# Kernel optimization log

Measured on AMD Instinct MI355X. Metric: run time of the kernel, lower is better.

## Reference

```python
import jax, jax.numpy as jnp
import numpy as np

K = 16  # knn_graph k, loop=True (self included since d(i,i)=0 is minimal)


def _knn_idx(pos, k):
    # exact kNN via pairwise squared distances; [N, k] neighbor indices
    sq = jnp.sum(pos * pos, axis=-1)
    d2 = sq[:, None] + sq[None, :] - 2.0 * (pos @ pos.T)  # [N, N]
    _, idx = jax.lax.top_k(-d2, k)
    return idx


def _pointnet_conv(x, pos, idx, Wa, ba, Wb, bb):
    # PointNetConv: msg = MLP(concat(x_j, pos_j - pos_i)), max-aggregate over neighbors
    rel = pos[idx] - pos[:, None, :]                    # [N, K, 3]
    m = jnp.concatenate([x[idx], rel], axis=-1)          # [N, K, Cin+3]
    h = jax.nn.relu(m @ Wa + ba) @ Wb + bb               # [N, K, Cout]
    return jnp.max(h, axis=1)                            # [N, Cout]


def setup_inputs() -> dict:
    key = jax.random.key(0)
    ks = jax.random.split(key, 13)
    N = 8192
    c1, c2, c3 = 64, 64, 128
    s = lambda fi: 1.0 / np.sqrt(fi)
    pos = jax.random.normal(ks[0], (N, 3), dtype=jnp.float32)
    return {
        "pos": pos,
        "W1a": jax.random.normal(ks[1], (3 + 3, c1), jnp.float32) * s(6),
        "b1a": jnp.zeros((c1,), jnp.float32),
        "W1b": jax.random.normal(ks[2], (c1, c1), jnp.float32) * s(c1),
        "b1b": jnp.zeros((c1,), jnp.float32),
        "W2a": jax.random.normal(ks[3], (c1 + 3, c2), jnp.float32) * s(c1 + 3),
        "b2a": jnp.zeros((c2,), jnp.float32),
        "W2b": jax.random.normal(ks[4], (c2, c2), jnp.float32) * s(c2),
        "b2b": jnp.zeros((c2,), jnp.float32),
        "W3a": jax.random.normal(ks[5], (c2 + 3, c3), jnp.float32) * s(c2 + 3),
        "b3a": jnp.zeros((c3,), jnp.float32),
        "W3b": jax.random.normal(ks[6], (c3, c3), jnp.float32) * s(c3),
        "b3b": jnp.zeros((c3,), jnp.float32),
    }


def reference(pos, W1a, b1a, W1b, b1b, W2a, b2a, W2b, b2b, W3a, b3a, W3b, b3b):
    idx = _knn_idx(pos, K)
    h1 = jax.nn.relu(_pointnet_conv(pos, pos, idx, W1a, b1a, W1b, b1b))
    h2 = jax.nn.relu(_pointnet_conv(h1, pos, idx, W2a, b2a, W2b, b2b))
    h3 = jax.nn.relu(_pointnet_conv(h2, pos, idx, W3a, b3a, W3b, b3b))
    return (h1, h2, h3)
```

## Files before the change

kernel.cpp:

```cpp
#include <hip/hip_runtime.h>
#include <math.h>

#define N_PTS 8192
#define KNN 16

typedef __attribute__((ext_vector_type(8))) short bf16x8;
typedef __attribute__((ext_vector_type(4))) float f32x4v;

__device__ __forceinline__ unsigned short f2bf(float f)
{
    unsigned u = __float_as_uint(f);
    u = u + 0x7fffu + ((u >> 16) & 1u);
    return (unsigned short)(u >> 16);
}
__device__ __forceinline__ unsigned pack2(float a, float b)
{
    return (unsigned)f2bf(a) | ((unsigned)f2bf(b) << 16);
}
__device__ __forceinline__ float rfl(float x)
{
    return __int_as_float(__builtin_amdgcn_readfirstlane(__float_as_int(x)));
}

__global__ __launch_bounds__(256) void prep_all(
    const float* __restrict__ pos, float4* __restrict__ pos4,
    const float* __restrict__ w1a, const float* __restrict__ w1b,
    const float* __restrict__ w2a, const float* __restrict__ w2b,
    const float* __restrict__ w3a, const float* __restrict__ w3b,
    uint4* __restrict__ dst)
{
    const int b = blockIdx.x;
    if (b < 88) {
        if (threadIdx.x >= 64) return;
        const float* Ws[6] = {w1a, w1b, w2a, w2b, w3a, w3b};
        const int Kd[6] = {6, 64, 67, 64, 67, 128};
        const int Nd[6] = {64, 64, 64, 64, 128, 128};
        const int start[7] = {0, 4, 12, 24, 32, 56, 88};
        int m = 0;
        while (b >= start[m + 1]) ++m;
        const int f  = b - start[m];
        const int NT = Nd[m] / 16;
        const int ks = f / NT, nt = f % NT;
        const int lane = threadIdx.x;
        const int c  = nt * 16 + (lane & 15);
        const int k0 = ks * 32 + (lane >> 4) * 8;
        const int K = Kd[m], N = Nd[m];
        const float* W = Ws[m];
        float v[8];
#pragma unroll
        for (int j = 0; j < 8; ++j) {
            const int kk = k0 + j;
            v[j] = (kk < K) ? W[kk * N + c] : 0.0f;
        }
        uint4 o;
        o.x = pack2(v[0], v[1]); o.y = pack2(v[2], v[3]);
        o.z = pack2(v[4], v[5]); o.w = pack2(v[6], v[7]);
        dst[b * 64 + lane] = o;
    } else {
        const int i = (b - 88) * 256 + threadIdx.x;
        const float x = pos[i * 3 + 0];
        const float y = pos[i * 3 + 1];
        const float z = pos[i * 3 + 2];
        pos4[i] = make_float4(x, y, z, fmaf(x, x, fmaf(y, y, z * z)));
    }
}

__device__ __forceinline__ unsigned sortkey(const float d2)
{
    unsigned u = __float_as_uint(d2);
    u ^= (unsigned)((int)u >> 31) | 0x80000000u;
    return u;
}
__device__ __forceinline__ float unkey(unsigned k)
{
    const unsigned u = (k & 0x80000000u) ? (k ^ 0x80000000u) : ~k;
    return __uint_as_float(u);
}

constexpr int CAP   = 128;
constexpr int QB    = 16;
constexpr int TILE  = 1024;
constexpr int NTL   = N_PTS / TILE;

__device__ __forceinline__ void stage_tile(const float4* src, float4* dst)
{
    __builtin_amdgcn_global_load_lds(
        (const __attribute__((address_space(1))) void*)src,
        (__attribute__((address_space(3))) void*)dst, 16, 0, 0);
}

__global__ __launch_bounds__(512) void knn_kernel(const float4* __restrict__ pos4,
                                                  int* __restrict__ idx_out)
{
    __shared__ float4 tile[2][TILE];
    __shared__ unsigned minkey[QB][64];
    __shared__ float Ts[QB];
    __shared__ unsigned long long surv[QB][CAP];
    __shared__ int scnt[QB];

    const int tid   = threadIdx.x;
    const int w     = tid >> 6;
    const int lane  = tid & 63;
    const int qbase = blockIdx.x * QB;

    if (tid < QB) scnt[tid] = 0;
    reinterpret_cast<unsigned*>(minkey)[tid]       = 0xFFFFFFFFu;
    reinterpret_cast<unsigned*>(minkey)[tid + 512] = 0xFFFFFFFFu;

    float qx[QB], qy[QB], qz[QB];
#pragma unroll
    for (int qi = 0; qi < QB; ++qi) {
        const float4 qp = pos4[qbase + qi];
        qx[qi] = rfl(-2.0f * qp.x);
        qy[qi] = rfl(-2.0f * qp.y);
        qz[qi] = rfl(-2.0f * qp.z);
    }

    const float4* src = pos4 + w * 128 + lane;
    float4* dst0 = &tile[0][w * 128];
    float4* dst1 = &tile[1][w * 128];

    float mn[QB];
#pragma unroll
    for (int qi = 0; qi < QB; ++qi) mn[qi] = 1e30f;

    stage_tile(src,      dst0);
    stage_tile(src + 64, dst0 + 64);
    __syncthreads();
#pragma unroll 1
    for (int t = 0; t < NTL - 1; ++t) {
        float4* nd = (t & 1) ? dst0 : dst1;
        stage_tile(src + (t + 1) * TILE,      nd);
        stage_tile(src + (t + 1) * TILE + 64, nd + 64);
        asm volatile("s_waitcnt vmcnt(2)" ::: "memory");
        __builtin_amdgcn_sched_barrier(0);
        const float4 p0 = tile[t & 1][w * 128 + lane];
        const float4 p1 = tile[t & 1][w * 128 + 64 + lane];
#pragma unroll
        for (int qi = 0; qi < QB; ++qi) {
            const float s0 = fmaf(qx[qi], p0.x, fmaf(qy[qi], p0.y, fmaf(qz[qi], p0.z, p0.w)));
            const float s1 = fmaf(qx[qi], p1.x, fmaf(qy[qi], p1.y, fmaf(qz[qi], p1.z, p1.w)));
            mn[qi] = fminf(mn[qi], fminf(s0, s1));
        }
    }
    {
        asm volatile("s_waitcnt vmcnt(0)" ::: "memory");
        __builtin_amdgcn_sched_barrier(0);
        const int t = NTL - 1;
        const float4 p0 = tile[t & 1][w * 128 + lane];
        const float4 p1 = tile[t & 1][w * 128 + 64 + lane];
#pragma unroll
        for (int qi = 0; qi < QB; ++qi) {
            const float s0 = fmaf(qx[qi], p0.x, fmaf(qy[qi], p0.y, fmaf(qz[qi], p0.z, p0.w)));
            const float s1 = fmaf(qx[qi], p1.x, fmaf(qy[qi], p1.y, fmaf(qz[qi], p1.z, p1.w)));
            mn[qi] = fminf(mn[qi], fminf(s0, s1));
        }
    }
#pragma unroll
    for (int qi = 0; qi < QB; ++qi) atomicMin(&minkey[qi][lane], sortkey(mn[qi]));
    __syncthreads();

#pragma unroll
    for (int k = 0; k < 2; ++k) {
        const int q = w * 2 + k;
        unsigned v = minkey[q][lane];
#pragma unroll
        for (int kk = 2; kk <= 64; kk <<= 1)
#pragma unroll
            for (int j = kk >> 1; j > 0; j >>= 1) {
                const unsigned o = __shfl_xor(v, j);
                const bool up = ((lane & kk) == 0);
                const bool lo = ((lane & j) == 0);
                v = (up == lo) ? min(v, o) : max(v, o);
            }
        if (lane == 15) Ts[q] = unkey(v);
    }
    __syncthreads();

    float T[QB];
#pragma unroll
    for (int qi = 0; qi < QB; ++qi) T[qi] = rfl(Ts[qi]);

    stage_tile(src,      dst0);
    stage_tile(src + 64, dst0 + 64);
#pragma unroll 1
    for (int t = 0; t < NTL - 1; ++t) {
        float4* nd = (t & 1) ? dst0 : dst1;
        stage_tile(src + (t + 1) * TILE,      nd);
        stage_tile(src + (t + 1) * TILE + 64, nd + 64);
        asm volatile("s_waitcnt vmcnt(2)" ::: "memory");
        __builtin_amdgcn_sched_barrier(0);
#pragma unroll
        for (int u = 0; u < 2; ++u) {
            const float4 p = tile[t & 1][w * 128 + u * 64 + lane];
            const int j = t * TILE + w * 128 + u * 64 + lane;
#pragma unroll
            for (int qi = 0; qi < QB; ++qi) {
                const float s = fmaf(qx[qi], p.x, fmaf(qy[qi], p.y, fmaf(qz[qi], p.z, p.w)));
                if (s <= T[qi]) {
                    const int slot = atomicAdd(&scnt[qi], 1);
                    if (slot < CAP)
                        surv[qi][slot] = ((unsigned long long)sortkey(s) << 32) | (unsigned)j;
                }
            }
        }
    }
    {
        asm volatile("s_waitcnt vmcnt(0)" ::: "memory");
        __builtin_amdgcn_sched_barrier(0);
        const int t = NTL - 1;
#pragma unroll
        for (int u = 0; u < 2; ++u) {
            const float4 p = tile[t & 1][w * 128 + u * 64 + lane];
            const int j = t * TILE + w * 128 + u * 64 + lane;
#pragma unroll
            for (int qi = 0; qi < QB; ++qi) {
                const float s = fmaf(qx[qi], p.x, fmaf(qy[qi], p.y, fmaf(qz[qi], p.z, p.w)));
                if (s <= T[qi]) {
                    const int slot = atomicAdd(&scnt[qi], 1);
                    if (slot < CAP)
                        surv[qi][slot] = ((unsigned long long)sortkey(s) << 32) | (unsigned)j;
                }
            }
        }
    }
    __syncthreads();

#pragma unroll
    for (int k = 0; k < 2; ++k) {
        const int q = w * 2 + k;
        const int n = min(scnt[q], CAP);
        const unsigned long long k0 = (lane < n) ? surv[q][lane] : ~0ull;
        const unsigned long long k1 = (lane + 64 < n) ? surv[q][lane + 64] : ~0ull;
        int r0 = 0, r1 = 0;
#pragma unroll 4
        for (int e = 0; e < n; ++e) {
            const unsigned long long ke = surv[q][e];
            r0 += (ke < k0) ? 1 : 0;
            r1 += (ke < k1) ? 1 : 0;
        }
        if (lane < n && r0 < KNN)
            idx_out[(qbase + q) * KNN + r0] = (int)(unsigned)(k0 & 0xFFFFFFFFu);
        if (lane + 64 < n && r1 < KNN)
            idx_out[(qbase + q) * KNN + r1] = (int)(unsigned)(k1 & 0xFFFFFFFFu);
    }
}

template <int CIN, int CMID, int COUT, int WM, int WN>
__global__ __launch_bounds__(256) void conv_mfma(
    const float* __restrict__ x, const float* __restrict__ pos,
    const int* __restrict__ idx,
    const uint4* __restrict__ fA, const float* __restrict__ ba,
    const uint4* __restrict__ fB, const float* __restrict__ bb,
    float* __restrict__ out)
{
    constexpr int PB  = 8, M = 128;
    constexpr int K1  = (CIN + 3 + 31) & ~31;
    constexpr int KS1 = K1 / 32;
    constexpr int KP1 = K1 + 8;
    constexpr int KS2 = CMID / 32;
    constexpr int KP2 = CMID + 8;
    constexpr int NT  = COUT / 16;
    constexpr int NTW = NT / WN;
    constexpr int MFW = (M / 16) / WM;
    constexpr int MSGS = M * KP1;
    constexpr int HBS  = M * KP2;
    constexpr int BUFS = (MSGS > HBS) ? MSGS : HBS;

    __shared__ int nbr[M];
    __shared__ __align__(16) unsigned short buf[BUFS];

    const int tid  = threadIdx.x;
    const int lane = tid & 63;
    const int w    = tid >> 6;
    const int wm   = w / WN, wn = w % WN;
    const int i0   = blockIdx.x * PB;

    if (tid < M) nbr[tid] = idx[i0 * KNN + tid];
    __syncthreads();

    if constexpr (CIN == 3) {
        if (tid < M) {
            const int row = tid, p = row >> 4, j = nbr[row];
            const float ax = pos[j * 3 + 0], ay = pos[j * 3 + 1], az = pos[j * 3 + 2];
            const float bx = pos[(i0 + p) * 3 + 0], by = pos[(i0 + p) * 3 + 1],
                        bz = pos[(i0 + p) * 3 + 2];
            uint4 c0;
            c0.x = pack2(ax, ay);
            c0.y = pack2(az, ax - bx);
            c0.z = pack2(ay - by, az - bz);
            c0.w = 0u;
            *reinterpret_cast<uint4*>(&buf[row * KP1 + 0])  = c0;
            const uint4 z = make_uint4(0, 0, 0, 0);
            *reinterpret_cast<uint4*>(&buf[row * KP1 + 8])  = z;
            *reinterpret_cast<uint4*>(&buf[row * KP1 + 16]) = z;
            *reinterpret_cast<uint4*>(&buf[row * KP1 + 24]) = z;
        }
    } else {
        const int row = tid >> 1, hh = tid & 1;
        const int j = nbr[row];
        const float* xr = x + j * CIN + hh * 32;
#pragma unroll
        for (int cc = 0; cc < 32; cc += 8) {
            const float4 f0 = *reinterpret_cast<const float4*>(xr + cc);
            const float4 f1 = *reinterpret_cast<const float4*>(xr + cc + 4);
            uint4 o;
            o.x = pack2(f0.x, f0.y); o.y = pack2(f0.z, f0.w);
            o.z = pack2(f1.x, f1.y); o.w = pack2(f1.z, f1.w);
            *reinterpret_cast<uint4*>(&buf[row * KP1 + hh * 32 + cc]) = o;
        }
        if (hh) {
            const int p = row >> 4;
            const float rx = pos[j * 3 + 0] - pos[(i0 + p) * 3 + 0];
            const float ry = pos[j * 3 + 1] - pos[(i0 + p) * 3 + 1];
            const float rz = pos[j * 3 + 2] - pos[(i0 + p) * 3 + 2];
            uint4 c0;
            c0.x = pack2(rx, ry);
            c0.y = pack2(rz, 0.0f);
            c0.z = 0u; c0.w = 0u;
            *reinterpret_cast<uint4*>(&buf[row * KP1 + 64]) = c0;
            const uint4 z = make_uint4(0, 0, 0, 0);
            *reinterpret_cast<uint4*>(&buf[row * KP1 + 72]) = z;
            *reinterpret_cast<uint4*>(&buf[row * KP1 + 80]) = z;
            *reinterpret_cast<uint4*>(&buf[row * KP1 + 88]) = z;
        }
    }
    __syncthreads();

    f32x4v acc[MFW][NTW];
    {
        uint4 b1[KS1][NTW];
#pragma unroll
        for (int ks = 0; ks < KS1; ++ks)
#pragma unroll
            for (int nt = 0; nt < NTW; ++nt)
                b1[ks][nt] = fA[(ks * NT + wn * NTW + nt) * 64 + lane];

#pragma unroll
        for (int mf = 0; mf < MFW; ++mf)
#pragma unroll
            for (int nt = 0; nt < NTW; ++nt) acc[mf][nt] = (f32x4v)0.0f;

#pragma unroll
        for (int mf = 0; mf < MFW; ++mf) {
            bf16x8 a[KS1];
#pragma unroll
            for (int ks = 0; ks < KS1; ++ks)
                a[ks] = *reinterpret_cast<const bf16x8*>(
                    &buf[((wm * MFW + mf) * 16 + (lane & 15)) * KP1 + ks * 32 + (lane >> 4) * 8]);
#pragma unroll
            for (int nt = 0; nt < NTW; ++nt)
#pragma unroll
                for (int ks = 0; ks < KS1; ++ks)
                    acc[mf][nt] = __builtin_amdgcn_mfma_f32_16x16x32_bf16(
                        a[ks], __builtin_bit_cast(bf16x8, b1[ks][nt]), acc[mf][nt], 0, 0, 0);
        }
    }
    __syncthreads();

    {
        float bav[NTW];
#pragma unroll
        for (int nt = 0; nt < NTW; ++nt) bav[nt] = ba[(wn * NTW + nt) * 16 + (lane & 15)];
#pragma unroll
        for (int mf = 0; mf < MFW; ++mf)
#pragma unroll
            for (int nt = 0; nt < NTW; ++nt)
#pragma unroll
                for (int r = 0; r < 4; ++r) {
                    const float v = fmaxf(acc[mf][nt][r] + bav[nt], 0.0f);
                    buf[((wm * MFW + mf) * 16 + (lane >> 4) * 4 + r) * KP2 +
                        (wn * NTW + nt) * 16 + (lane & 15)] = f2bf(v);
                }
    }
    __syncthreads();

    {
        uint4 b2[KS2][NTW];
#pragma unroll
        for (int ks = 0; ks < KS2; ++ks)
#pragma unroll
            for (int nt = 0; nt < NTW; ++nt)
                b2[ks][nt] = fB[(ks * NT + wn * NTW + nt) * 64 + lane];

        f32x4v acc2[MFW][NTW];
#pragma unroll
        for (int mf = 0; mf < MFW; ++mf)
#pragma unroll
            for (int nt = 0; nt < NTW; ++nt) acc2[mf][nt] = (f32x4v)0.0f;

#pragma unroll
        for (int mf = 0; mf < MFW; ++mf) {
            bf16x8 a[KS2];
#pragma unroll
            for (int ks = 0; ks < KS2; ++ks)
                a[ks] = *reinterpret_cast<const bf16x8*>(
                    &buf[((wm * MFW + mf) * 16 + (lane & 15)) * KP2 + ks * 32 + (lane >> 4) * 8]);
#pragma unroll
            for (int nt = 0; nt < NTW; ++nt)
#pragma unroll
                for (int ks = 0; ks < KS2; ++ks)
                    acc2[mf][nt] = __builtin_amdgcn_mfma_f32_16x16x32_bf16(
                        a[ks], __builtin_bit_cast(bf16x8, b2[ks][nt]), acc2[mf][nt], 0, 0, 0);
        }

        float bbv[NTW];
#pragma unroll
        for (int nt = 0; nt < NTW; ++nt) bbv[nt] = bb[(wn * NTW + nt) * 16 + (lane & 15)];

#pragma unroll
        for (int mf = 0; mf < MFW; ++mf)
#pragma unroll
            for (int nt = 0; nt < NTW; ++nt) {
                const f32x4v t = acc2[mf][nt];
                float m0 = fmaxf(fmaxf(t[0], t[1]), fmaxf(t[2], t[3]));
                m0 = fmaxf(m0, __shfl_xor(m0, 16));
                m0 = fmaxf(m0, __shfl_xor(m0, 32));
                const float v = fmaxf(m0 + bbv[nt], 0.0f);
                if (lane < 16)
                    out[(i0 + wm * MFW + mf) * COUT + (wn * NTW + nt) * 16 + lane] = v;
            }
    }
}

extern "C" void kernel_launch(void* const* d_in, const int* in_sizes, int n_in,
                              void* d_out, int out_size, void* d_ws, size_t ws_size,
                              hipStream_t stream)
{
    const float* pos = (const float*)d_in[0];
    const float* W1a = (const float*)d_in[1];
    const float* b1a = (const float*)d_in[2];
    const float* W1b = (const float*)d_in[3];
    const float* b1b = (const float*)d_in[4];
    const float* W2a = (const float*)d_in[5];
    const float* b2a = (const float*)d_in[6];
    const float* W2b = (const float*)d_in[7];
    const float* b2b = (const float*)d_in[8];
    const float* W3a = (const float*)d_in[9];
    const float* b3a = (const float*)d_in[10];
    const float* W3b = (const float*)d_in[11];
    const float* b3b = (const float*)d_in[12];

    float* out = (float*)d_out;
    float* h1 = out;
    float* h2 = out + N_PTS * 64;
    float* h3 = out + N_PTS * 128;

    int*   idx     = (int*)d_ws;
    uint4* wsFrags = (uint4*)((char*)d_ws + N_PTS * KNN * 4);

    float4* pos4 = (float4*)h3;

    prep_all<<<120, 256, 0, stream>>>(pos, pos4, W1a, W1b, W2a, W2b, W3a, W3b, wsFrags);
    knn_kernel<<<N_PTS / QB, 512, 0, stream>>>(pos4, idx);

    const uint4* fW1a = wsFrags + 0 * 64;
    const uint4* fW1b = wsFrags + 4 * 64;
    const uint4* fW2a = wsFrags + 12 * 64;
    const uint4* fW2b = wsFrags + 24 * 64;
    const uint4* fW3a = wsFrags + 32 * 64;
    const uint4* fW3b = wsFrags + 56 * 64;

    conv_mfma<3, 64, 64, 4, 1><<<N_PTS / 8, 256, 0, stream>>>(
        pos, pos, idx, fW1a, b1a, fW1b, b1b, h1);
    conv_mfma<64, 64, 64, 4, 1><<<N_PTS / 8, 256, 0, stream>>>(
        h1, pos, idx, fW2a, b2a, fW2b, b2b, h2);
    conv_mfma<64, 128, 128, 2, 2><<<N_PTS / 8, 256, 0, stream>>>(
        h2, pos, idx, fW3a, b3a, fW3b, b3b, h3);
}
```

Measured before the change: 74.24 us.

## Halve kNN query block, triple-buffer tiles, and early-out candidate filtering

Cuts the kNN kernel to 8 queries and 512-point tiles per block, which doubles the block count and adds a launch-bounds occupancy hint. Tile staging moves from double to triple buffering, so loads run two tiles ahead of compute. The filtering pass now computes all query scores first and branches only when some query passes its threshold, aiming to skip the per-query atomic path in the common case. In exchange, the position array is streamed twice per block across twice as many blocks, so global/L2 traffic doubles.

```diff
diff --git a/kernel.cpp b/kernel.cpp
--- a/kernel.cpp
+++ b/kernel.cpp
@@ -78,8 +78,8 @@
 }
 
 constexpr int CAP   = 128;
-constexpr int QB    = 16;
-constexpr int TILE  = 1024;
+constexpr int QB    = 8;
+constexpr int TILE  = 512;
 constexpr int NTL   = N_PTS / TILE;
 
 __device__ __forceinline__ void stage_tile(const float4* src, float4* dst)
@@ -89,10 +89,10 @@
         (__attribute__((address_space(3))) void*)dst, 16, 0, 0);
 }
 
-__global__ __launch_bounds__(512) void knn_kernel(const float4* __restrict__ pos4,
-                                                  int* __restrict__ idx_out)
-{
-    __shared__ float4 tile[2][TILE];
+__global__ __launch_bounds__(512, 8) void knn_kernel(const float4* __restrict__ pos4,
+                                                     int* __restrict__ idx_out)
+{
+    __shared__ float4 tile[3][TILE];
     __shared__ unsigned minkey[QB][64];
     __shared__ float Ts[QB];
     __shared__ unsigned long long surv[QB][CAP];
@@ -104,8 +104,7 @@
     const int qbase = blockIdx.x * QB;
 
     if (tid < QB) scnt[tid] = 0;
-    reinterpret_cast<unsigned*>(minkey)[tid]       = 0xFFFFFFFFu;
-    reinterpret_cast<unsigned*>(minkey)[tid + 512] = 0xFFFFFFFFu;
+    reinterpret_cast<unsigned*>(minkey)[tid] = 0xFFFFFFFFu;
 
     float qx[QB], qy[QB], qz[QB];
 #pragma unroll
@@ -116,54 +115,46 @@
         qz[qi] = rfl(-2.0f * qp.z);
     }
 
-    const float4* src = pos4 + w * 128 + lane;
-    float4* dst0 = &tile[0][w * 128];
-    float4* dst1 = &tile[1][w * 128];
+    const float4* src = pos4 + w * 64 + lane;
 
     float mn[QB];
 #pragma unroll
     for (int qi = 0; qi < QB; ++qi) mn[qi] = 1e30f;
 
-    stage_tile(src,      dst0);
-    stage_tile(src + 64, dst0 + 64);
+    stage_tile(src + 0 * TILE, &tile[0][w * 64]);
+    stage_tile(src + 1 * TILE, &tile[1][w * 64]);
     __syncthreads();
 #pragma unroll 1
-    for (int t = 0; t < NTL - 1; ++t) {
-        float4* nd = (t & 1) ? dst0 : dst1;
-        stage_tile(src + (t + 1) * TILE,      nd);
-        stage_tile(src + (t + 1) * TILE + 64, nd + 64);
+    for (int t = 0; t < NTL - 2; ++t) {
+        stage_tile(src + (t + 2) * TILE, &tile[(t + 2) % 3][w * 64]);
         asm volatile("s_waitcnt vmcnt(2)" ::: "memory");
         __builtin_amdgcn_sched_barrier(0);
-        const float4 p0 = tile[t & 1][w * 128 + lane];
-        const float4 p1 = tile[t & 1][w * 128 + 64 + lane];
+        const float4 p = tile[t % 3][w * 64 + lane];
 #pragma unroll
         for (int qi = 0; qi < QB; ++qi) {
-            const float s0 = fmaf(qx[qi], p0.x, fmaf(qy[qi], p0.y, fmaf(qz[qi], p0.z, p0.w)));
-            const float s1 = fmaf(qx[qi], p1.x, fmaf(qy[qi], p1.y, fmaf(qz[qi], p1.z, p1.w)));
-            mn[qi] = fminf(mn[qi], fminf(s0, s1));
-        }
-    }
+            const float s = fmaf(qx[qi], p.x, fmaf(qy[qi], p.y, fmaf(qz[qi], p.z, p.w)));
+            mn[qi] = fminf(mn[qi], s);
+        }
+    }
+#pragma unroll
+    for (int tt = 0; tt < 2; ++tt) {
+        if (tt == 0) asm volatile("s_waitcnt vmcnt(1)" ::: "memory");
+        else         asm volatile("s_waitcnt vmcnt(0)" ::: "memory");
+        __builtin_amdgcn_sched_barrier(0);
+        const int t = NTL - 2 + tt;
+        const float4 p = tile[t % 3][w * 64 + lane];
+#pragma unroll
+        for (int qi = 0; qi < QB; ++qi) {
+            const float s = fmaf(qx[qi], p.x, fmaf(qy[qi], p.y, fmaf(qz[qi], p.z, p.w)));
+            mn[qi] = fminf(mn[qi], s);
+        }
+    }
+#pragma unroll
+    for (int qi = 0; qi < QB; ++qi) atomicMin(&minkey[qi][lane], sortkey(mn[qi]));
+    __syncthreads();
+
     {
-        asm volatile("s_waitcnt vmcnt(0)" ::: "memory");
-        __builtin_amdgcn_sched_barrier(0);
-        const int t = NTL - 1;
-        const float4 p0 = tile[t & 1][w * 128 + lane];
-        const float4 p1 = tile[t & 1][w * 128 + 64 + lane];
-#pragma unroll
-        for (int qi = 0; qi < QB; ++qi) {
-            const float s0 = fmaf(qx[qi], p0.x, fmaf(qy[qi], p0.y, fmaf(qz[qi], p0.z, p0.w)));
-            const float s1 = fmaf(qx[qi], p1.x, fmaf(qy[qi], p1.y, fmaf(qz[qi], p1.z, p1.w)));
-            mn[qi] = fminf(mn[qi], fminf(s0, s1));
-        }
-    }
-#pragma unroll
-    for (int qi = 0; qi < QB; ++qi) atomicMin(&minkey[qi][lane], sortkey(mn[qi]));
-    __syncthreads();
-
-#pragma unroll
-    for (int k = 0; k < 2; ++k) {
-        const int q = w * 2 + k;
-        unsigned v = minkey[q][lane];
+        unsigned v = minkey[w][lane];
 #pragma unroll
         for (int kk = 2; kk <= 64; kk <<= 1)
 #pragma unroll
@@ -173,7 +164,7 @@
                 const bool lo = ((lane & j) == 0);
                 v = (up == lo) ? min(v, o) : max(v, o);
             }
-        if (lane == 15) Ts[q] = unkey(v);
+        if (lane == 15) Ts[w] = unkey(v);
     }
     __syncthreads();
 
@@ -181,54 +172,61 @@
 #pragma unroll
     for (int qi = 0; qi < QB; ++qi) T[qi] = rfl(Ts[qi]);
 
-    stage_tile(src,      dst0);
-    stage_tile(src + 64, dst0 + 64);
+    stage_tile(src + 0 * TILE, &tile[0][w * 64]);
+    stage_tile(src + 1 * TILE, &tile[1][w * 64]);
 #pragma unroll 1
-    for (int t = 0; t < NTL - 1; ++t) {
-        float4* nd = (t & 1) ? dst0 : dst1;
-        stage_tile(src + (t + 1) * TILE,      nd);
-        stage_tile(src + (t + 1) * TILE + 64, nd + 64);
+    for (int t = 0; t < NTL - 2; ++t) {
+        stage_tile(src + (t + 2) * TILE, &tile[(t + 2) % 3][w * 64]);
         asm volatile("s_waitcnt vmcnt(2)" ::: "memory");
         __builtin_amdgcn_sched_barrier(0);
-#pragma unroll
-        for (int u = 0; u < 2; ++u) {
-            const float4 p = tile[t & 1][w * 128 + u * 64 + lane];
-            const int j = t * TILE + w * 128 + u * 64 + lane;
-#pragma unroll
-            for (int qi = 0; qi < QB; ++qi) {
-                const float s = fmaf(qx[qi], p.x, fmaf(qy[qi], p.y, fmaf(qz[qi], p.z, p.w)));
-                if (s <= T[qi]) {
+        const float4 p = tile[t % 3][w * 64 + lane];
+        const int j = t * TILE + w * 64 + lane;
+        float s[QB];
+        bool hit = false;
+#pragma unroll
+        for (int qi = 0; qi < QB; ++qi) {
+            s[qi] = fmaf(qx[qi], p.x, fmaf(qy[qi], p.y, fmaf(qz[qi], p.z, p.w)));
+            hit = hit | (s[qi] <= T[qi]);
+        }
+        if (__builtin_expect(hit, 0)) {
+#pragma unroll
+            for (int qi = 0; qi < QB; ++qi)
+                if (s[qi] <= T[qi]) {
                     const int slot = atomicAdd(&scnt[qi], 1);
                     if (slot < CAP)
-                        surv[qi][slot] = ((unsigned long long)sortkey(s) << 32) | (unsigned)j;
+                        surv[qi][slot] = ((unsigned long long)sortkey(s[qi]) << 32) | (unsigned)j;
                 }
-            }
-        }
-    }
-    {
-        asm volatile("s_waitcnt vmcnt(0)" ::: "memory");
+        }
+    }
+#pragma unroll
+    for (int tt = 0; tt < 2; ++tt) {
+        if (tt == 0) asm volatile("s_waitcnt vmcnt(1)" ::: "memory");
+        else         asm volatile("s_waitcnt vmcnt(0)" ::: "memory");
         __builtin_amdgcn_sched_barrier(0);
-        const int t = NTL - 1;
-#pragma unroll
-        for (int u = 0; u < 2; ++u) {
-            const float4 p = tile[t & 1][w * 128 + u * 64 + lane];
-            const int j = t * TILE + w * 128 + u * 64 + lane;
-#pragma unroll
-            for (int qi = 0; qi < QB; ++qi) {
-                const float s = fmaf(qx[qi], p.x, fmaf(qy[qi], p.y, fmaf(qz[qi], p.z, p.w)));
-                if (s <= T[qi]) {
+        const int t = NTL - 2 + tt;
+        const float4 p = tile[t % 3][w * 64 + lane];
+        const int j = t * TILE + w * 64 + lane;
+        float s[QB];
+        bool hit = false;
+#pragma unroll
+        for (int qi = 0; qi < QB; ++qi) {
+            s[qi] = fmaf(qx[qi], p.x, fmaf(qy[qi], p.y, fmaf(qz[qi], p.z, p.w)));
+            hit = hit | (s[qi] <= T[qi]);
+        }
+        if (__builtin_expect(hit, 0)) {
+#pragma unroll
+            for (int qi = 0; qi < QB; ++qi)
+                if (s[qi] <= T[qi]) {
                     const int slot = atomicAdd(&scnt[qi], 1);
                     if (slot < CAP)
-                        surv[qi][slot] = ((unsigned long long)sortkey(s) << 32) | (unsigned)j;
+                        surv[qi][slot] = ((unsigned long long)sortkey(s[qi]) << 32) | (unsigned)j;
                 }
-            }
-        }
-    }
-    __syncthreads();
-
-#pragma unroll
-    for (int k = 0; k < 2; ++k) {
-        const int q = w * 2 + k;
+        }
+    }
+    __syncthreads();
+
+    {
+        const int q = w;
         const int n = min(scnt[q], CAP);
         const unsigned long long k0 = (lane < n) ? surv[q][lane] : ~0ull;
         const unsigned long long k1 = (lane + 64 < n) ? surv[q][lane + 64] : ~0ull;
```

Measured after the change: 77.99 us. 5.0% more time.

## Precompute per-point first-layer projections and fuse them into previous conv epilogue

Applied to the files above, without the earlier changes.

Splits the first linear layer of each PointNetConv algebraically into a per-source-point term (x_j and pos_j times Wa, plus bias) and a per-center term (pos_i times the rel rows of Wa). The per-point term is computed once per point, in prep for layer 1 and in the previous conv's epilogue for later layers, and stored as bf16. The conv kernel then only gathers these vectors, subtracts the center term and applies relu. This removes the first MFMA GEMM over N*K messages, adding a scalar FMA epilogue, extra scratch buffers placed in output and workspace, and extra bf16 rounding of the intermediate.

```diff
diff --git a/kernel.cpp b/kernel.cpp
--- a/kernel.cpp
+++ b/kernel.cpp
@@ -17,6 +17,10 @@
 {
     return (unsigned)f2bf(a) | ((unsigned)f2bf(b) << 16);
 }
+__device__ __forceinline__ float bf2f(unsigned short h)
+{
+    return __uint_as_float((unsigned)h << 16);
+}
 __device__ __forceinline__ float rfl(float x)
 {
     return __int_as_float(__builtin_amdgcn_readfirstlane(__float_as_int(x)));
@@ -24,18 +28,19 @@
 
 __global__ __launch_bounds__(256) void prep_all(
     const float* __restrict__ pos, float4* __restrict__ pos4,
-    const float* __restrict__ w1a, const float* __restrict__ w1b,
-    const float* __restrict__ w2a, const float* __restrict__ w2b,
-    const float* __restrict__ w3a, const float* __restrict__ w3b,
+    unsigned short* __restrict__ v1,
+    const float* __restrict__ w1a, const float* __restrict__ b1a,
+    const float* __restrict__ w1b, const float* __restrict__ w2b,
+    const float* __restrict__ w3b,
     uint4* __restrict__ dst)
 {
     const int b = blockIdx.x;
-    if (b < 88) {
+    if (b < 48) {
         if (threadIdx.x >= 64) return;
-        const float* Ws[6] = {w1a, w1b, w2a, w2b, w3a, w3b};
-        const int Kd[6] = {6, 64, 67, 64, 67, 128};
-        const int Nd[6] = {64, 64, 64, 64, 128, 128};
-        const int start[7] = {0, 4, 12, 24, 32, 56, 88};
+        const float* Ws[3] = {w1b, w2b, w3b};
+        const int Kd[3] = {64, 64, 128};
+        const int Nd[3] = {64, 64, 128};
+        const int start[4] = {0, 8, 16, 48};
         int m = 0;
         while (b >= start[m + 1]) ++m;
         const int f  = b - start[m];
@@ -44,24 +49,43 @@
         const int lane = threadIdx.x;
         const int c  = nt * 16 + (lane & 15);
         const int k0 = ks * 32 + (lane >> 4) * 8;
-        const int K = Kd[m], N = Nd[m];
+        const int N = Nd[m];
         const float* W = Ws[m];
         float v[8];
 #pragma unroll
-        for (int j = 0; j < 8; ++j) {
-            const int kk = k0 + j;
-            v[j] = (kk < K) ? W[kk * N + c] : 0.0f;
-        }
+        for (int j = 0; j < 8; ++j) v[j] = W[(k0 + j) * N + c];
         uint4 o;
         o.x = pack2(v[0], v[1]); o.y = pack2(v[2], v[3]);
         o.z = pack2(v[4], v[5]); o.w = pack2(v[6], v[7]);
         dst[b * 64 + lane] = o;
-    } else {
-        const int i = (b - 88) * 256 + threadIdx.x;
+    } else if (b < 80) {
+        const int i = (b - 48) * 256 + threadIdx.x;
         const float x = pos[i * 3 + 0];
         const float y = pos[i * 3 + 1];
         const float z = pos[i * 3 + 2];
         pos4[i] = make_float4(x, y, z, fmaf(x, x, fmaf(y, y, z * z)));
+    } else {
+        const int i = (b - 80) * 256 + threadIdx.x;
+        const float px = pos[i * 3 + 0], py = pos[i * 3 + 1], pz = pos[i * 3 + 2];
+#pragma unroll
+        for (int c8 = 0; c8 < 64; c8 += 8) {
+            unsigned o[4];
+#pragma unroll
+            for (int d2 = 0; d2 < 4; ++d2) {
+                float r[2];
+#pragma unroll
+                for (int e = 0; e < 2; ++e) {
+                    const int c = c8 + d2 * 2 + e;
+                    float acc = b1a[c];
+                    acc = fmaf(px, w1a[0 * 64 + c] + w1a[3 * 64 + c], acc);
+                    acc = fmaf(py, w1a[1 * 64 + c] + w1a[4 * 64 + c], acc);
+                    acc = fmaf(pz, w1a[2 * 64 + c] + w1a[5 * 64 + c], acc);
+                    r[e] = acc;
+                }
+                o[d2] = pack2(r[0], r[1]);
+            }
+            *reinterpret_cast<uint4*>(v1 + i * 64 + c8) = make_uint4(o[0], o[1], o[2], o[3]);
+        }
     }
 }
 
@@ -233,7 +257,6 @@
         const unsigned long long k0 = (lane < n) ? surv[q][lane] : ~0ull;
         const unsigned long long k1 = (lane + 64 < n) ? surv[q][lane + 64] : ~0ull;
         int r0 = 0, r1 = 0;
-#pragma unroll 4
         for (int e = 0; e < n; ++e) {
             const unsigned long long ke = surv[q][e];
             r0 += (ke < k0) ? 1 : 0;
@@ -246,29 +269,25 @@
     }
 }
 
-template <int CIN, int CMID, int COUT, int WM, int WN>
-__global__ __launch_bounds__(256) void conv_mfma(
-    const float* __restrict__ x, const float* __restrict__ pos,
+template <int CMID, int COUT, int WM, int WN, int VNEXT>
+__global__ __launch_bounds__(256) void conv_fused(
+    const unsigned short* __restrict__ v, const float* __restrict__ pos,
     const int* __restrict__ idx,
-    const uint4* __restrict__ fA, const float* __restrict__ ba,
+    const float* __restrict__ WaRel,
     const uint4* __restrict__ fB, const float* __restrict__ bb,
-    float* __restrict__ out)
+    const float* __restrict__ Wnext, const float* __restrict__ bnext,
+    float* __restrict__ out, unsigned short* __restrict__ vout)
 {
     constexpr int PB  = 8, M = 128;
-    constexpr int K1  = (CIN + 3 + 31) & ~31;
-    constexpr int KS1 = K1 / 32;
-    constexpr int KP1 = K1 + 8;
+    constexpr int KP2 = CMID + 8;
     constexpr int KS2 = CMID / 32;
-    constexpr int KP2 = CMID + 8;
     constexpr int NT  = COUT / 16;
     constexpr int NTW = NT / WN;
     constexpr int MFW = (M / 16) / WM;
-    constexpr int MSGS = M * KP1;
-    constexpr int HBS  = M * KP2;
-    constexpr int BUFS = (MSGS > HBS) ? MSGS : HBS;
 
     __shared__ int nbr[M];
-    __shared__ __align__(16) unsigned short buf[BUFS];
+    __shared__ float ubuf[PB][CMID];
+    __shared__ __align__(16) unsigned short hbuf[M * KP2];
 
     const int tid  = threadIdx.x;
     const int lane = tid & 63;
@@ -277,104 +296,40 @@
     const int i0   = blockIdx.x * PB;
 
     if (tid < M) nbr[tid] = idx[i0 * KNN + tid];
-    __syncthreads();
-
-    if constexpr (CIN == 3) {
-        if (tid < M) {
-            const int row = tid, p = row >> 4, j = nbr[row];
-            const float ax = pos[j * 3 + 0], ay = pos[j * 3 + 1], az = pos[j * 3 + 2];
-            const float bx = pos[(i0 + p) * 3 + 0], by = pos[(i0 + p) * 3 + 1],
-                        bz = pos[(i0 + p) * 3 + 2];
-            uint4 c0;
-            c0.x = pack2(ax, ay);
-            c0.y = pack2(az, ax - bx);
-            c0.z = pack2(ay - by, az - bz);
-            c0.w = 0u;
-            *reinterpret_cast<uint4*>(&buf[row * KP1 + 0])  = c0;
-            const uint4 z = make_uint4(0, 0, 0, 0);
-            *reinterpret_cast<uint4*>(&buf[row * KP1 + 8])  = z;
-            *reinterpret_cast<uint4*>(&buf[row * KP1 + 16]) = z;
-            *reinterpret_cast<uint4*>(&buf[row * KP1 + 24]) = z;
-        }
-    } else {
+    for (int e = tid; e < PB * CMID; e += 256) {
+        const int pt = e / CMID, c = e % CMID;
+        float u = pos[(i0 + pt) * 3 + 0] * WaRel[c];
+        u = fmaf(pos[(i0 + pt) * 3 + 1], WaRel[CMID + c], u);
+        u = fmaf(pos[(i0 + pt) * 3 + 2], WaRel[2 * CMID + c], u);
+        ubuf[pt][c] = u;
+    }
+    __syncthreads();
+
+    {
         const int row = tid >> 1, hh = tid & 1;
-        const int j = nbr[row];
-        const float* xr = x + j * CIN + hh * 32;
-#pragma unroll
-        for (int cc = 0; cc < 32; cc += 8) {
-            const float4 f0 = *reinterpret_cast<const float4*>(xr + cc);
-            const float4 f1 = *reinterpret_cast<const float4*>(xr + cc + 4);
-            uint4 o;
-            o.x = pack2(f0.x, f0.y); o.y = pack2(f0.z, f0.w);
-            o.z = pack2(f1.x, f1.y); o.w = pack2(f1.z, f1.w);
-            *reinterpret_cast<uint4*>(&buf[row * KP1 + hh * 32 + cc]) = o;
-        }
-        if (hh) {
-            const int p = row >> 4;
-            const float rx = pos[j * 3 + 0] - pos[(i0 + p) * 3 + 0];
-            const float ry = pos[j * 3 + 1] - pos[(i0 + p) * 3 + 1];
-            const float rz = pos[j * 3 + 2] - pos[(i0 + p) * 3 + 2];
-            uint4 c0;
-            c0.x = pack2(rx, ry);
-            c0.y = pack2(rz, 0.0f);
-            c0.z = 0u; c0.w = 0u;
-            *reinterpret_cast<uint4*>(&buf[row * KP1 + 64]) = c0;
-            const uint4 z = make_uint4(0, 0, 0, 0);
-            *reinterpret_cast<uint4*>(&buf[row * KP1 + 72]) = z;
-            *reinterpret_cast<uint4*>(&buf[row * KP1 + 80]) = z;
-            *reinterpret_cast<uint4*>(&buf[row * KP1 + 88]) = z;
-        }
-    }
-    __syncthreads();
-
-    f32x4v acc[MFW][NTW];
-    {
-        uint4 b1[KS1][NTW];
-#pragma unroll
-        for (int ks = 0; ks < KS1; ++ks)
-#pragma unroll
-            for (int nt = 0; nt < NTW; ++nt)
-                b1[ks][nt] = fA[(ks * NT + wn * NTW + nt) * 64 + lane];
-
-#pragma unroll
-        for (int mf = 0; mf < MFW; ++mf)
-#pragma unroll
-            for (int nt = 0; nt < NTW; ++nt) acc[mf][nt] = (f32x4v)0.0f;
-
-#pragma unroll
-        for (int mf = 0; mf < MFW; ++mf) {
-            bf16x8 a[KS1];
-#pragma unroll
-            for (int ks = 0; ks < KS1; ++ks)
-                a[ks] = *reinterpret_cast<const bf16x8*>(
-                    &buf[((wm * MFW + mf) * 16 + (lane & 15)) * KP1 + ks * 32 + (lane >> 4) * 8]);
-#pragma unroll
-            for (int nt = 0; nt < NTW; ++nt)
-#pragma unroll
-                for (int ks = 0; ks < KS1; ++ks)
-                    acc[mf][nt] = __builtin_amdgcn_mfma_f32_16x16x32_bf16(
-                        a[ks], __builtin_bit_cast(bf16x8, b1[ks][nt]), acc[mf][nt], 0, 0, 0);
-        }
-    }
-    __syncthreads();
-
-    {
-        float bav[NTW];
-#pragma unroll
-        for (int nt = 0; nt < NTW; ++nt) bav[nt] = ba[(wn * NTW + nt) * 16 + (lane & 15)];
-#pragma unroll
-        for (int mf = 0; mf < MFW; ++mf)
-#pragma unroll
-            for (int nt = 0; nt < NTW; ++nt)
-#pragma unroll
-                for (int r = 0; r < 4; ++r) {
-                    const float v = fmaxf(acc[mf][nt][r] + bav[nt], 0.0f);
-                    buf[((wm * MFW + mf) * 16 + (lane >> 4) * 4 + r) * KP2 +
-                        (wn * NTW + nt) * 16 + (lane & 15)] = f2bf(v);
-                }
-    }
-    __syncthreads();
-
+        const int j = nbr[row], pt = row >> 4;
+        const int cb = hh * (CMID / 2);
+#pragma unroll
+        for (int cc = 0; cc < CMID / 2; cc += 8) {
+            const uint4 vv = *reinterpret_cast<const uint4*>(v + j * CMID + cb + cc);
+            const unsigned dw[4] = {vv.x, vv.y, vv.z, vv.w};
+            unsigned o[4];
+#pragma unroll
+            for (int d2 = 0; d2 < 4; ++d2) {
+                const int c = cb + cc + d2 * 2;
+                const float flo = __uint_as_float(dw[d2] << 16);
+                const float fhi = __uint_as_float(dw[d2] & 0xffff0000u);
+                const float rlo = fmaxf(flo - ubuf[pt][c],     0.0f);
+                const float rhi = fmaxf(fhi - ubuf[pt][c + 1], 0.0f);
+                o[d2] = pack2(rlo, rhi);
+            }
+            *reinterpret_cast<uint4*>(&hbuf[row * KP2 + cb + cc]) =
+                make_uint4(o[0], o[1], o[2], o[3]);
+        }
+    }
+    __syncthreads();
+
+    float outv[MFW][NTW];
     {
         uint4 b2[KS2][NTW];
 #pragma unroll
@@ -395,7 +350,7 @@
 #pragma unroll
             for (int ks = 0; ks < KS2; ++ks)
                 a[ks] = *reinterpret_cast<const bf16x8*>(
-                    &buf[((wm * MFW + mf) * 16 + (lane & 15)) * KP2 + ks * 32 + (lane >> 4) * 8]);
+                    &hbuf[((wm * MFW + mf) * 16 + (lane & 15)) * KP2 + ks * 32 + (lane >> 4) * 8]);
 #pragma unroll
             for (int nt = 0; nt < NTW; ++nt)
 #pragma unroll
@@ -416,10 +371,52 @@
                 float m0 = fmaxf(fmaxf(t[0], t[1]), fmaxf(t[2], t[3]));
                 m0 = fmaxf(m0, __shfl_xor(m0, 16));
                 m0 = fmaxf(m0, __shfl_xor(m0, 32));
-                const float v = fmaxf(m0 + bbv[nt], 0.0f);
-                if (lane < 16)
-                    out[(i0 + wm * MFW + mf) * COUT + (wn * NTW + nt) * 16 + lane] = v;
-            }
+                outv[mf][nt] = fmaxf(m0 + bbv[nt], 0.0f);
+            }
+    }
+    __syncthreads();
+
+#pragma unroll
+    for (int mf = 0; mf < MFW; ++mf)
+#pragma unroll
+        for (int nt = 0; nt < NTW; ++nt) {
+            if (lane < 16) {
+                const int pt = wm * MFW + mf;
+                const int c  = (wn * NTW + nt) * 16 + lane;
+                out[(i0 + pt) * COUT + c] = outv[mf][nt];
+                if constexpr (VNEXT > 0) hbuf[pt * KP2 + c] = f2bf(outv[mf][nt]);
+            }
+        }
+
+    if constexpr (VNEXT > 0) {
+        __syncthreads();
+        constexpr int CPT = VNEXT / 32;
+        const int pt = tid >> 5;
+        const int c0 = (tid & 31) * CPT;
+        float acc[CPT];
+#pragma unroll
+        for (int e = 0; e < CPT; ++e) acc[e] = bnext[c0 + e];
+        for (int k = 0; k < COUT; ++k) {
+            const float hk = bf2f(hbuf[pt * KP2 + k]);
+#pragma unroll
+            for (int e = 0; e < CPT; ++e)
+                acc[e] = fmaf(hk, Wnext[k * VNEXT + c0 + e], acc[e]);
+        }
+#pragma unroll
+        for (int d = 0; d < 3; ++d) {
+            const float pd = pos[(i0 + pt) * 3 + d];
+#pragma unroll
+            for (int e = 0; e < CPT; ++e)
+                acc[e] = fmaf(pd, Wnext[(COUT + d) * VNEXT + c0 + e], acc[e]);
+        }
+        if constexpr (CPT == 2) {
+            *reinterpret_cast<unsigned*>(vout + (i0 + pt) * VNEXT + c0) = pack2(acc[0], acc[1]);
+        } else {
+            uint2 o;
+            o.x = pack2(acc[0], acc[1]);
+            o.y = pack2(acc[2], acc[3]);
+            *reinterpret_cast<uint2*>(vout + (i0 + pt) * VNEXT + c0) = o;
+        }
     }
 }
 
@@ -446,25 +443,25 @@
     float* h2 = out + N_PTS * 64;
     float* h3 = out + N_PTS * 128;
 
-    int*   idx     = (int*)d_ws;
-    uint4* wsFrags = (uint4*)((char*)d_ws + N_PTS * KNN * 4);
-
-    float4* pos4 = (float4*)h3;
-
-    prep_all<<<120, 256, 0, stream>>>(pos, pos4, W1a, W1b, W2a, W2b, W3a, W3b, wsFrags);
+    int*            idx     = (int*)d_ws;
+    uint4*          wsFrags = (uint4*)((char*)d_ws + 524288);
+    unsigned short* v3      = (unsigned short*)((char*)d_ws + 589824);
+
+    float4*         pos4 = (float4*)h3;
+    unsigned short* v1   = (unsigned short*)((char*)h3 + 131072);
+    unsigned short* v2   = (unsigned short*)((char*)h3 + 1179648);
+
+    prep_all<<<112, 256, 0, stream>>>(pos, pos4, v1, W1a, b1a, W1b, W2b, W3b, wsFrags);
     knn_kernel<<<N_PTS / QB, 512, 0, stream>>>(pos4, idx);
 
-    const uint4* fW1a = wsFrags + 0 * 64;
-    const uint4* fW1b = wsFrags + 4 * 64;
-    const uint4* fW2a = wsFrags + 12 * 64;
-    const uint4* fW2b = wsFrags + 24 * 64;
-    const uint4* fW3a = wsFrags + 32 * 64;
-    const uint4* fW3b = wsFrags + 56 * 64;
-
-    conv_mfma<3, 64, 64, 4, 1><<<N_PTS / 8, 256, 0, stream>>>(
-        pos, pos, idx, fW1a, b1a, fW1b, b1b, h1);
-    conv_mfma<64, 64, 64, 4, 1><<<N_PTS / 8, 256, 0, stream>>>(
-        h1, pos, idx, fW2a, b2a, fW2b, b2b, h2);
-    conv_mfma<64, 128, 128, 2, 2><<<N_PTS / 8, 256, 0, stream>>>(
-        h2, pos, idx, fW3a, b3a, fW3b, b3b, h3);
-}
+    const uint4* fW1b = wsFrags + 0 * 64;
+    const uint4* fW2b = wsFrags + 8 * 64;
+    const uint4* fW3b = wsFrags + 16 * 64;
+
+    conv_fused<64, 64, 4, 1, 64><<<N_PTS / 8, 256, 0, stream>>>(
+        v1, pos, idx, W1a + 3 * 64, fW1b, b1b, W2a, b2a, h1, v2);
+    conv_fused<64, 64, 4, 1, 128><<<N_PTS / 8, 256, 0, stream>>>(
+        v2, pos, idx, W2a + 64 * 64, fW2b, b2b, W3a, b3a, h2, v3);
+    conv_fused<128, 128, 2, 2, 0><<<N_PTS / 8, 256, 0, stream>>>(
+        v3, pos, idx, W3a + 64 * 128, fW3b, b3b, nullptr, nullptr, h3, nullptr);
+}
```

Result: slower. 81.54 us (+9.8%).
